# Kernel tuning notes

Hardware: AMD Instinct MI355X
Metric: run time of the kernel (lower is better)

## Reference

```python
import jax, jax.numpy as jnp
import numpy as np
from jax import lax

W_MAX = 8
STEP = 1
LEAK = 2
KSIZE = (W_MAX - 1) * (STEP + LEAK)  # 21 = kernel size, padding, and fodep
THETA = 80
FODEP = KSIZE
OUT_CH = 1
NEURONS = 1024


def make_w_kernel_table():
    # StepFireLeak response table: [w_max, ksize], flipped in time
    w_idx = np.arange(W_MAX, dtype=np.float32)[:, None]
    t_idx = np.arange(KSIZE, dtype=np.float32)[None, :]
    w_step = np.maximum(np.floor(1.0 + t_idx / STEP), 0.0)
    w_leak = np.maximum(np.ceil(w_idx + ((w_idx - 1.0) * STEP - t_idx) / LEAK), 0.0)
    table = np.minimum(w_step, w_leak).astype(np.int32)[:, ::-1]
    return jnp.asarray(np.ascontiguousarray(table))


def setup_inputs() -> dict:
    key = jax.random.key(0)
    k1, k2 = jax.random.split(key)
    B, C, S, T = 64, 1, 784, 500
    input_spikes = (jax.random.uniform(k1, (B, C, S, T)) < 0.05).astype(jnp.float32)
    # integer synaptic weights in [0, w_max)
    weight = jax.random.randint(k2, (OUT_CH * NEURONS, C * S), 0, W_MAX, dtype=jnp.int32)
    return {"input_spikes": input_spikes, "weight": weight}


def reference(input_spikes, weight):
    B, C, S, T = input_spikes.shape
    x = input_spikes.reshape(B, C * S, T)
    # expand integer weights into response kernels: [out, in, ksize]
    table = make_w_kernel_table().astype(jnp.float32)
    kern = table[weight]
    pot = lax.conv_general_dilated(
        x, kern, window_strides=(1,), padding=[(KSIZE, KSIZE)],
        dimension_numbers=("NCH", "OIH", "NCH"))
    pot = jnp.rint(pot).astype(jnp.int32)
    Tp = pot.shape[-1]  # T + ksize + 1
    pot = pot.reshape(B, OUT_CH, NEURONS, Tp)
    pot_t = jnp.transpose(pot, (3, 0, 1, 2))  # [Tp, B, C, N]

    def step(dep, p):  # dep: [B, C] int32, p: [B, C, N]
        winner = jnp.argmax(p, axis=-1)  # [B, C]
        val = jnp.take_along_axis(p, winner[..., None], axis=-1)[..., 0]
        cond = ((val > THETA) & (dep == 0)).astype(jnp.int32)  # min_depression == 0
        winners_t = jax.nn.one_hot(winner, NEURONS, dtype=jnp.int32) * cond[..., None]
        new_dep = jnp.maximum(0, dep + cond * (FODEP + 1) - 1)
        return new_dep, winners_t

    dep0 = jnp.zeros((B, OUT_CH), dtype=jnp.int32)
    _, winners = lax.scan(step, dep0, pot_t)  # [Tp, B, C, N]
    return jnp.transpose(winners, (1, 2, 3, 0))  # [B, C, N, Tp]
```

## Files before the change

kernel.cpp:

```cpp
#include <hip/hip_runtime.h>

#define B_DIM 64
#define S_DIM 784
#define T_DIM 500
#define N_DIM 1024
#define TP    522
#define KS    21
#define THETA 80
#define NCHUNK 8
#define CH    66
#define LISTCAP 128
#define SW64  13
#define BMSTRIDE 16

__global__ void k_prep(const int* __restrict__ w, unsigned char* __restrict__ wt9) {
  unsigned idx = blockIdx.x * 256 + threadIdx.x;
  if (idx < S_DIM * N_DIM) {
    unsigned s = idx >> 10, n = idx & 1023;
    int wv = w[n * S_DIM + s];
    wt9[idx] = wv ? (unsigned char)(9 * (wv - 1)) : (unsigned char)63;
  }
}

__global__ void __launch_bounds__(1024)
k_bitmap(const float* __restrict__ x, unsigned long long* __restrict__ bm) {
  __shared__ unsigned long long s_m[S_DIM];
  const int tid = threadIdx.x;
  const int wave = tid >> 6, lane = tid & 63;
  const int b = blockIdx.y;
  const int t0 = blockIdx.x * 64;
  const int t = t0 + lane;
  const bool tok = (t < T_DIM);
  const float* xb = x + (size_t)b * S_DIM * T_DIM;

  for (int s = wave; s < S_DIM; s += 16) {
    float v = tok ? xb[(size_t)s * T_DIM + t] : 0.0f;
    unsigned long long m = __ballot(v != 0.0f);
    if (lane == 0) s_m[s] = m;
  }
  __syncthreads();

  if (wave < SW64) {
    const int sbase = wave * 64;
    const unsigned long long mask_s =
        (sbase + lane < S_DIM) ? s_m[sbase + lane] : 0ull;
    unsigned long long* dst = bm + ((size_t)b * 512 + t0) * BMSTRIDE + wave;
    for (int tl = 0; tl < 64; ++tl) {
      unsigned long long wrd = __ballot((mask_s >> tl) & 1ull);
      if (lane == 0) dst[(size_t)tl * BMSTRIDE] = wrd;
    }
  }
}

__global__ void __launch_bounds__(1024, 8)
k_main(const unsigned char* __restrict__ wt9,
       const unsigned long long* __restrict__ bm,
       unsigned* __restrict__ red) {
  __shared__ unsigned short s_list[87][LISTCAP];
  __shared__ int s_cnt[87];
  __shared__ unsigned smax[CH];

  const int tid = threadIdx.x;
  const int b = blockIdx.y;
  const int lo = blockIdx.x * CH;
  const int hi = min(TP - 1, lo + CH - 1);
  const int t0 = max(0, lo - KS);
  const int n_emit = hi - lo + 1;
  const int nt_in = min(hi, T_DIM - 1) - t0 + 1;

  for (int i = tid; i < nt_in; i += 1024) s_cnt[i] = 0;
  for (int i = tid; i < n_emit; i += 1024) smax[i] = 0u;
  __syncthreads();

  const unsigned long long* bmb = bm + ((size_t)b * 512 + t0) * BMSTRIDE;
  const int ntask = nt_in * SW64;
  for (int task = tid; task < ntask; task += 1024) {
    const int li = task / SW64;
    const int sw = task - li * SW64;
    unsigned long long w = bmb[(size_t)li * BMSTRIDE + sw];
    if (w) {
      int c = __popcll(w);
      int pos = atomicAdd(&s_cnt[li], c);
      const int sb = sw * 64;
      while (w) {
        int j = __builtin_ctzll(w);
        if (pos < LISTCAP) s_list[li][pos] = (unsigned short)(sb + j);
        ++pos;
        w &= (w - 1);
      }
    }
  }
  __syncthreads();

  int ring[KS + 1];
  #pragma unroll
  for (int i = 0; i <= KS; ++i) ring[i] = 0;

  const unsigned invn = (unsigned)(1023 - tid);

  for (int t = t0; t <= hi; ++t) {
    if (t >= lo) {
      unsigned key = ((unsigned)ring[0] << 10) | invn;
      #pragma unroll
      for (int off = 32; off > 0; off >>= 1) {
        unsigned o = __shfl_xor(key, off, 64);
        key = key > o ? key : o;
      }
      if ((tid & 63) == 0) atomicMax(&smax[t - lo], key);
    }

    if (t < T_DIM) {
      const int li = t - t0;
      const int cnt = __builtin_amdgcn_readfirstlane(min(s_cnt[li], LISTCAP));
      const unsigned short* lp = &s_list[li][0];
      unsigned long long ca = 0, cb = 0;
      int i = 0;
      for (; i + 1 < cnt; i += 2) {
        unsigned ia = ((unsigned)lp[i] << 10) + tid;
        unsigned ib = ((unsigned)lp[i + 1] << 10) + tid;
        ca += 1ull << wt9[ia];
        cb += 1ull << wt9[ib];
      }
      if (i < cnt) ca += 1ull << wt9[((unsigned)lp[i] << 10) + tid];
      const unsigned long long c = ca + cb;

      const int c1 = (int)(c & 511), c2 = (int)((c >> 9) & 511), c3 = (int)((c >> 18) & 511),
                c4 = (int)((c >> 27) & 511), c5 = (int)((c >> 36) & 511),
                c6 = (int)((c >> 45) & 511), c7 = (int)((c >> 54) & 511);
      const int S7 = c7, S6 = S7 + c6, S5 = S6 + c5, S4 = S5 + c4,
                S3 = S4 + c3, S2 = S3 + c2, S1 = S2 + c1;
      const int O1 = c1, O3 = O1 + c3, O5 = O3 + c5, O7 = O5 + c7;
      const int E2 = c2, E4 = E2 + c4, E6 = E4 + c6;
      const int O31 = O3 - O1, O51 = O5 - O1, O71 = O7 - O1,
                O73 = O7 - O3, O75 = O7 - O5;
      const int E62 = E6 - E2, E64 = E6 - E4;
      int acc = S1;        ring[1]  += acc;
      acc += S2;           ring[2]  += acc;
      acc += S3 - O1;      ring[3]  += acc;
      acc += S4 - E2;      ring[4]  += acc;
      acc += S5 - O31;     ring[5]  += acc;
      acc += S6 - E4;      ring[6]  += acc;
      acc += S7 - O51;     ring[7]  += acc;
      acc -= E62;          ring[8]  += acc;
      acc -= O71;          ring[9]  += acc;
      acc -= E62;          ring[10] += acc;
      acc -= O73;          ring[11] += acc;
      acc -= E62;          ring[12] += acc;
      acc -= O73;          ring[13] += acc;
      acc -= E64;          ring[14] += acc;
      acc -= O73;          ring[15] += acc;
      acc -= E64;          ring[16] += acc;
      acc -= O75;          ring[17] += acc;
      acc -= E64;          ring[18] += acc;
      acc -= O75;          ring[19] += acc;
                           ring[20] += acc;
      acc -= O75;          ring[21] += acc;
    }

    #pragma unroll
    for (int i = 0; i < KS; ++i) ring[i] = ring[i + 1];
    ring[KS] = 0;
  }

  __syncthreads();
  for (int i = tid; i < n_emit; i += 1024)
    red[(unsigned)b * TP + (unsigned)(lo + i)] = smax[i];
}

__global__ void __launch_bounds__(256)
k_scan(const unsigned* __restrict__ red, unsigned* __restrict__ winner) {
  const int wv = (int)((blockIdx.x * 256 + threadIdx.x) >> 6);
  const int lane = threadIdx.x & 63;
  if (wv >= B_DIM) return;
  const unsigned* r = red + wv * TP;
  unsigned* wn = winner + wv * TP;
  int dep = 0;
  for (int base = 0; base < TP; base += 64) {
    const int nt = min(64, TP - base);
    unsigned key = (lane < nt) ? r[base + lane] : 0u;
    unsigned w = 0;
    for (int j = 0; j < nt; ++j) {
      unsigned kj = __shfl(key, j, 64);
      bool cond = ((int)(kj >> 10) > THETA) && (dep == 0);
      if (cond && lane == j) w = 1024u - (kj & 1023u);
      dep += cond ? 22 : 0;
      dep = max(0, dep - 1);
    }
    if (lane < nt) wn[base + lane] = w;
  }
}

__global__ void __launch_bounds__(256)
k_fill(const unsigned* __restrict__ winner, int* __restrict__ out) {
  const int n = blockIdx.x;
  const int b = blockIdx.y;
  const unsigned* wn = winner + b * TP;
  int* o = out + ((size_t)b * N_DIM + n) * TP;
  const unsigned target = (unsigned)(n + 1);
  int2* o2 = (int2*)o;
  for (int i = threadIdx.x; i < TP / 2; i += 256) {
    int2 v;
    v.x = (wn[2 * i]     == target) ? 1 : 0;
    v.y = (wn[2 * i + 1] == target) ? 1 : 0;
    o2[i] = v;
  }
}

extern "C" void kernel_launch(void* const* d_in, const int* in_sizes, int n_in,
                              void* d_out, int out_size, void* d_ws, size_t ws_size,
                              hipStream_t stream) {
  const float* x = (const float*)d_in[0];
  const int* wgt = (const int*)d_in[1];
  int* out = (int*)d_out;

  unsigned char* wt9      = (unsigned char*)d_ws;
  unsigned long long* bm  = (unsigned long long*)((char*)d_ws + 802816);
  unsigned* red           = (unsigned*)((char*)d_ws + 802816 + 4194304);
  unsigned* winner        = (unsigned*)((char*)d_ws + 802816 + 4194304 + 133632);

  k_prep<<<3136, 256, 0, stream>>>(wgt, wt9);
  k_bitmap<<<dim3(8, B_DIM), 1024, 0, stream>>>(x, bm);
  k_main<<<dim3(NCHUNK, B_DIM), 1024, 0, stream>>>(wt9, bm, red);
  k_scan<<<(B_DIM * 64 + 255) / 256, 256, 0, stream>>>(red, winner);
  k_fill<<<dim3(N_DIM, B_DIM), 256, 0, stream>>>(winner, out);
}
```

Measured before the change: 615.9 us.

## Drop halo recomputation by spilling head/tail partial potentials and fixing chunk boundaries

Result: faster. 563.9 us (-8.5%).

```diff
diff --git a/kernel.cpp b/kernel.cpp
--- a/kernel.cpp
+++ b/kernel.cpp
@@ -13,12 +13,12 @@
 #define SW64  13
 #define BMSTRIDE 16
 
-__global__ void k_prep(const int* __restrict__ w, unsigned char* __restrict__ wt9) {
+__global__ void k_prep(const int* __restrict__ w, unsigned char* __restrict__ wt8) {
   unsigned idx = blockIdx.x * 256 + threadIdx.x;
   if (idx < S_DIM * N_DIM) {
     unsigned s = idx >> 10, n = idx & 1023;
     int wv = w[n * S_DIM + s];
-    wt9[idx] = wv ? (unsigned char)(9 * (wv - 1)) : (unsigned char)63;
+    wt8[idx] = wv ? (unsigned char)(8 * (wv - 1)) : (unsigned char)56;
   }
 }
 
@@ -52,10 +52,174 @@
   }
 }
 
+#define SPIKE_RING_BODY(LI)                                                          \
+  {                                                                                  \
+    const int cnt = __builtin_amdgcn_readfirstlane(min(s_cnt[(LI)], LISTCAP));       \
+    const unsigned short* lp = &s_list[(LI)][0];                                     \
+    unsigned long long ca = 0, cb = 0;                                               \
+    int i = 0;                                                                       \
+    for (; i + 1 < cnt; i += 2) {                                                    \
+      unsigned ia = ((unsigned)lp[i] << 10) + tid;                                   \
+      unsigned ib = ((unsigned)lp[i + 1] << 10) + tid;                               \
+      ca += 1ull << wt8[ia];                                                         \
+      cb += 1ull << wt8[ib];                                                         \
+    }                                                                                \
+    if (i < cnt) ca += 1ull << wt8[((unsigned)lp[i] << 10) + tid];                   \
+    const unsigned long long c = ca + cb;                                            \
+    const unsigned clo = (unsigned)c, chi = (unsigned)(c >> 32);                     \
+    const int c1 = (int)(clo & 255), c2 = (int)((clo >> 8) & 255),                   \
+              c3 = (int)((clo >> 16) & 255), c4 = (int)(clo >> 24);                  \
+    const int c5 = (int)(chi & 255), c6 = (int)((chi >> 8) & 255),                   \
+              c7 = (int)((chi >> 16) & 255);                                         \
+    const int S7 = c7, S6 = S7 + c6, S5 = S6 + c5, S4 = S5 + c4,                     \
+              S3 = S4 + c3, S2 = S3 + c2, S1 = S2 + c1;                              \
+    const int O1 = c1, O3 = O1 + c3, O5 = O3 + c5, O7 = O5 + c7;                     \
+    const int E2 = c2, E4 = E2 + c4, E6 = E4 + c6;                                   \
+    const int O31 = O3 - O1, O51 = O5 - O1, O71 = O7 - O1,                           \
+              O73 = O7 - O3, O75 = O7 - O5;                                          \
+    const int E62 = E6 - E2, E64 = E6 - E4;                                          \
+    int acc = S1;        ring[1]  += acc;                                            \
+    acc += S2;           ring[2]  += acc;                                            \
+    acc += S3 - O1;      ring[3]  += acc;                                            \
+    acc += S4 - E2;      ring[4]  += acc;                                            \
+    acc += S5 - O31;     ring[5]  += acc;                                            \
+    acc += S6 - E4;      ring[6]  += acc;                                            \
+    acc += S7 - O51;     ring[7]  += acc;                                            \
+    acc -= E62;          ring[8]  += acc;                                            \
+    acc -= O71;          ring[9]  += acc;                                            \
+    acc -= E62;          ring[10] += acc;                                            \
+    acc -= O73;          ring[11] += acc;                                            \
+    acc -= E62;          ring[12] += acc;                                            \
+    acc -= O73;          ring[13] += acc;                                            \
+    acc -= E64;          ring[14] += acc;                                            \
+    acc -= O73;          ring[15] += acc;                                            \
+    acc -= E64;          ring[16] += acc;                                            \
+    acc -= O75;          ring[17] += acc;                                            \
+    acc -= E64;          ring[18] += acc;                                            \
+    acc -= O75;          ring[19] += acc;                                            \
+                         ring[20] += acc;                                            \
+    acc -= O75;          ring[21] += acc;                                            \
+  }
+
+#define RING_SHIFT()                                                                 \
+  {                                                                                  \
+    _Pragma("unroll")                                                                \
+    for (int q = 0; q < KS; ++q) ring[q] = ring[q + 1];                              \
+    ring[KS] = 0;                                                                    \
+  }
+
 __global__ void __launch_bounds__(1024, 8)
-k_main(const unsigned char* __restrict__ wt9,
-       const unsigned long long* __restrict__ bm,
-       unsigned* __restrict__ red) {
+k_mainA(const unsigned char* __restrict__ wt8,
+        const unsigned long long* __restrict__ bm,
+        unsigned* __restrict__ red,
+        unsigned short* __restrict__ headb,
+        unsigned short* __restrict__ tailb) {
+  __shared__ unsigned short s_list[CH][LISTCAP];
+  __shared__ int s_cnt[CH];
+  __shared__ unsigned smax[CH - KS];
+
+  const int tid = threadIdx.x;
+  const int b = blockIdx.y;
+  const int ck = blockIdx.x;
+  const int lo = ck * CH;
+  const int hi = min(TP - 1, lo + CH - 1);
+  const int nt_in = min(hi, T_DIM - 1) - lo + 1;
+  const int n_full = hi - lo - (KS - 1);
+
+  for (int i = tid; i < nt_in; i += 1024) s_cnt[i] = 0;
+  for (int i = tid; i < n_full; i += 1024) smax[i] = 0u;
+  __syncthreads();
+
+  const unsigned long long* bmb = bm + ((size_t)b * 512 + lo) * BMSTRIDE;
+  const int ntask = nt_in * SW64;
+  for (int task = tid; task < ntask; task += 1024) {
+    const int li = task / SW64;
+    const int sw = task - li * SW64;
+    unsigned long long w = bmb[(size_t)li * BMSTRIDE + sw];
+    if (w) {
+      int cc = __popcll(w);
+      int pos = atomicAdd(&s_cnt[li], cc);
+      const int sb = sw * 64;
+      while (w) {
+        int j = __builtin_ctzll(w);
+        if (pos < LISTCAP) s_list[li][pos] = (unsigned short)(sb + j);
+        ++pos;
+        w &= (w - 1);
+      }
+    }
+  }
+  __syncthreads();
+
+  int ring[KS + 1];
+  #pragma unroll
+  for (int i = 0; i <= KS; ++i) ring[i] = 0;
+
+  const unsigned invn = (unsigned)(1023 - tid);
+  unsigned short* hb = headb + ((size_t)b * NCHUNK + ck) * (KS * 1024) + tid;
+
+  for (int t = lo; t <= hi; ++t) {
+    const int j = t - lo;
+    if (j < KS) {
+      hb[(size_t)j * 1024] = (unsigned short)ring[0];
+    } else {
+      unsigned key = ((unsigned)ring[0] << 10) | invn;
+      #pragma unroll
+      for (int off = 32; off > 0; off >>= 1) {
+        unsigned o = __shfl_xor(key, off, 64);
+        key = key > o ? key : o;
+      }
+      if ((tid & 63) == 0) atomicMax(&smax[j - KS], key);
+    }
+
+    if (t < T_DIM) {
+      const int li = t - lo;
+      SPIKE_RING_BODY(li)
+    }
+    RING_SHIFT()
+  }
+
+  if (ck < NCHUNK - 1) {
+    unsigned short* tb = tailb + ((size_t)b * NCHUNK + ck) * (KS * 1024) + tid;
+    #pragma unroll
+    for (int j2 = 0; j2 < KS; ++j2) tb[(size_t)j2 * 1024] = (unsigned short)ring[j2];
+  }
+
+  __syncthreads();
+  for (int i = tid; i < n_full; i += 1024)
+    red[(unsigned)b * TP + (unsigned)(lo + KS + i)] = smax[i];
+}
+
+__global__ void __launch_bounds__(1024)
+k_fix(const unsigned short* __restrict__ headb,
+      const unsigned short* __restrict__ tailb,
+      unsigned* __restrict__ red) {
+  __shared__ unsigned smax[KS];
+  const int tid = threadIdx.x;
+  const int b = blockIdx.y, ck = blockIdx.x;
+  const int lo = ck * CH;
+  if (tid < KS) smax[tid] = 0u;
+  __syncthreads();
+  const size_t base = ((size_t)b * NCHUNK + ck) * (KS * 1024) + tid;
+  const unsigned invn = (unsigned)(1023 - tid);
+  for (int j = 0; j < KS; ++j) {
+    int v = headb[base + (size_t)j * 1024];
+    if (ck > 0) v += tailb[base - (size_t)KS * 1024 + (size_t)j * 1024];
+    unsigned key = ((unsigned)v << 10) | invn;
+    #pragma unroll
+    for (int off = 32; off > 0; off >>= 1) {
+      unsigned o = __shfl_xor(key, off, 64);
+      key = key > o ? key : o;
+    }
+    if ((tid & 63) == 0) atomicMax(&smax[j], key);
+  }
+  __syncthreads();
+  if (tid < KS) red[(unsigned)b * TP + (unsigned)(lo + tid)] = smax[tid];
+}
+
+__global__ void __launch_bounds__(1024, 8)
+k_mainH(const unsigned char* __restrict__ wt8,
+        const unsigned long long* __restrict__ bm,
+        unsigned* __restrict__ red) {
   __shared__ unsigned short s_list[87][LISTCAP];
   __shared__ int s_cnt[87];
   __shared__ unsigned smax[CH];
@@ -79,8 +243,8 @@
     const int sw = task - li * SW64;
     unsigned long long w = bmb[(size_t)li * BMSTRIDE + sw];
     if (w) {
-      int c = __popcll(w);
-      int pos = atomicAdd(&s_cnt[li], c);
+      int cc = __popcll(w);
+      int pos = atomicAdd(&s_cnt[li], cc);
       const int sb = sw * 64;
       while (w) {
         int j = __builtin_ctzll(w);
@@ -108,58 +272,11 @@
       }
       if ((tid & 63) == 0) atomicMax(&smax[t - lo], key);
     }
-
     if (t < T_DIM) {
       const int li = t - t0;
-      const int cnt = __builtin_amdgcn_readfirstlane(min(s_cnt[li], LISTCAP));
-      const unsigned short* lp = &s_list[li][0];
-      unsigned long long ca = 0, cb = 0;
-      int i = 0;
-      for (; i + 1 < cnt; i += 2) {
-        unsigned ia = ((unsigned)lp[i] << 10) + tid;
-        unsigned ib = ((unsigned)lp[i + 1] << 10) + tid;
-        ca += 1ull << wt9[ia];
-        cb += 1ull << wt9[ib];
-      }
-      if (i < cnt) ca += 1ull << wt9[((unsigned)lp[i] << 10) + tid];
-      const unsigned long long c = ca + cb;
-
-      const int c1 = (int)(c & 511), c2 = (int)((c >> 9) & 511), c3 = (int)((c >> 18) & 511),
-                c4 = (int)((c >> 27) & 511), c5 = (int)((c >> 36) & 511),
-                c6 = (int)((c >> 45) & 511), c7 = (int)((c >> 54) & 511);
-      const int S7 = c7, S6 = S7 + c6, S5 = S6 + c5, S4 = S5 + c4,
-                S3 = S4 + c3, S2 = S3 + c2, S1 = S2 + c1;
-      const int O1 = c1, O3 = O1 + c3, O5 = O3 + c5, O7 = O5 + c7;
-      const int E2 = c2, E4 = E2 + c4, E6 = E4 + c6;
-      const int O31 = O3 - O1, O51 = O5 - O1, O71 = O7 - O1,
-                O73 = O7 - O3, O75 = O7 - O5;
-      const int E62 = E6 - E2, E64 = E6 - E4;
-      int acc = S1;        ring[1]  += acc;
-      acc += S2;           ring[2]  += acc;
-      acc += S3 - O1;      ring[3]  += acc;
-      acc += S4 - E2;      ring[4]  += acc;
-      acc += S5 - O31;     ring[5]  += acc;
-      acc += S6 - E4;      ring[6]  += acc;
-      acc += S7 - O51;     ring[7]  += acc;
-      acc -= E62;          ring[8]  += acc;
-      acc -= O71;          ring[9]  += acc;
-      acc -= E62;          ring[10] += acc;
-      acc -= O73;          ring[11] += acc;
-      acc -= E62;          ring[12] += acc;
-      acc -= O73;          ring[13] += acc;
-      acc -= E64;          ring[14] += acc;
-      acc -= O73;          ring[15] += acc;
-      acc -= E64;          ring[16] += acc;
-      acc -= O75;          ring[17] += acc;
-      acc -= E64;          ring[18] += acc;
-      acc -= O75;          ring[19] += acc;
-                           ring[20] += acc;
-      acc -= O75;          ring[21] += acc;
-    }
-
-    #pragma unroll
-    for (int i = 0; i < KS; ++i) ring[i] = ring[i + 1];
-    ring[KS] = 0;
+      SPIKE_RING_BODY(li)
+    }
+    RING_SHIFT()
   }
 
   __syncthreads();
@@ -213,14 +330,31 @@
   const int* wgt = (const int*)d_in[1];
   int* out = (int*)d_out;
 
-  unsigned char* wt9      = (unsigned char*)d_ws;
-  unsigned long long* bm  = (unsigned long long*)((char*)d_ws + 802816);
-  unsigned* red           = (unsigned*)((char*)d_ws + 802816 + 4194304);
-  unsigned* winner        = (unsigned*)((char*)d_ws + 802816 + 4194304 + 133632);
-
-  k_prep<<<3136, 256, 0, stream>>>(wgt, wt9);
+  const size_t OFF_BM   = 802816;
+  const size_t OFF_RED  = OFF_BM + 4194304;
+  const size_t OFF_WIN  = OFF_RED + 133632;
+  const size_t OFF_HEAD = OFF_WIN + 133632;
+  const size_t HT_SZ    = (size_t)B_DIM * NCHUNK * KS * 1024 * 2;
+  const size_t OFF_TAIL = OFF_HEAD + HT_SZ;
+  const size_t NEED_SPLIT = OFF_TAIL + HT_SZ;
+
+  unsigned char* wt8      = (unsigned char*)d_ws;
+  unsigned long long* bm  = (unsigned long long*)((char*)d_ws + OFF_BM);
+  unsigned* red           = (unsigned*)((char*)d_ws + OFF_RED);
+  unsigned* winner        = (unsigned*)((char*)d_ws + OFF_WIN);
+
+  k_prep<<<3136, 256, 0, stream>>>(wgt, wt8);
   k_bitmap<<<dim3(8, B_DIM), 1024, 0, stream>>>(x, bm);
-  k_main<<<dim3(NCHUNK, B_DIM), 1024, 0, stream>>>(wt9, bm, red);
+
+  if (ws_size >= NEED_SPLIT) {
+    unsigned short* headb = (unsigned short*)((char*)d_ws + OFF_HEAD);
+    unsigned short* tailb = (unsigned short*)((char*)d_ws + OFF_TAIL);
+    k_mainA<<<dim3(NCHUNK, B_DIM), 1024, 0, stream>>>(wt8, bm, red, headb, tailb);
+    k_fix<<<dim3(NCHUNK, B_DIM), 1024, 0, stream>>>(headb, tailb, red);
+  } else {
+    k_mainH<<<dim3(NCHUNK, B_DIM), 1024, 0, stream>>>(wt8, bm, red);
+  }
+
   k_scan<<<(B_DIM * 64 + 255) / 256, 256, 0, stream>>>(red, winner);
   k_fill<<<dim3(N_DIM, B_DIM), 256, 0, stream>>>(winner, out);
 }
```
